# Optimization experiments

Measured on AMD Instinct MI355X. Metric: run time of the kernel, lower is better.

The kernel has to match this reference:

```python
import jax, jax.numpy as jnp
import numpy as np

NUM_HEADS = 16
HEAD_DIM = 64  # hidden_size / num_heads


def setup_inputs() -> dict:
    key = jax.random.key(0)
    ks = jax.random.split(key, 20)
    B, S, H, K = 16, 1024, 1024, 64
    d = {"hidden_states": jax.random.normal(ks[0], (B, S, H), jnp.float32)}
    i = 1
    for p in ("q", "k", "v", "o"):
        d["W" + p] = jax.random.normal(ks[i], (H, H), jnp.float32) * (1.0 / np.sqrt(H)); i += 1
        d["b" + p] = jax.random.normal(ks[i], (H,), jnp.float32) * 0.02; i += 1
        d["LM" + p] = jax.random.normal(ks[i], (H, K), jnp.float32) * (1.0 / np.sqrt(K)); i += 1
        d["RM" + p] = jax.random.normal(ks[i], (K, H), jnp.float32) * (1.0 / np.sqrt(H)); i += 1
        d["F" + p] = jnp.ones((H,), jnp.float32)
    d["task"] = 0
    return d


def _proj(x, W, b, LM, RM, F):
    # RG weight reconstruction: weight = LM @ RM + W  (task==0 branch)
    w = LM @ RM + W  # [h_out, h_in]
    y = jnp.einsum("bsi,oi->bso", x, w) + b
    return y * F  # SFG per-channel scaling


def reference(hidden_states, Wq, bq, LMq, RMq, Fq, Wk, bk, LMk, RMk, Fk,
              Wv, bv, LMv, RMv, Fv, Wo, bo, LMo, RMo, Fo, task):
    B, S, H = hidden_states.shape
    nh, hd = NUM_HEADS, HEAD_DIM
    q = _proj(hidden_states, Wq, bq, LMq, RMq, Fq).reshape(B, S, nh, hd)
    k = _proj(hidden_states, Wk, bk, LMk, RMk, Fk).reshape(B, S, nh, hd)
    v = _proj(hidden_states, Wv, bv, LMv, RMv, Fv).reshape(B, S, nh, hd)
    scores = jnp.einsum("bqhd,bkhd->bhqk", q, k) / np.sqrt(hd).astype(np.float32)
    probs = jax.nn.softmax(scores, axis=-1)  # attn_dropout rate = 0.0
    ctx = jnp.einsum("bhqk,bkhd->bqhd", probs, v).reshape(B, S, H)
    out = _proj(ctx, Wo, bo, LMo, RMo, Fo)  # proj_dropout rate = 0.0
    return out
```

## Files before the change

kernel.cpp:

```cpp
#include <hip/hip_runtime.h>
#include <cstdint>
#include <cstddef>

typedef short short8 __attribute__((ext_vector_type(8)));
typedef float f32x4 __attribute__((ext_vector_type(4)));
typedef float f32x16 __attribute__((ext_vector_type(16)));
typedef unsigned short us4 __attribute__((ext_vector_type(4)));

__device__ __forceinline__ unsigned short f2bf(float f) {
  unsigned int u = __float_as_uint(f);
  unsigned int r = (u + 0x7fffu + ((u >> 16) & 1u)) >> 16;
  return (unsigned short)r;
}
__device__ __forceinline__ float exp2_fast(float x) {
  return __builtin_amdgcn_exp2f(x);
}
__device__ __forceinline__ float max3f(float a, float b, float c) {
  return fmaxf(fmaxf(a, b), c);
}
__device__ __forceinline__ unsigned int cvt_pk_bf16(float a, float b) {
  unsigned int d;
  asm("v_cvt_pk_bf16_f32 %0, %1, %2" : "=v"(d) : "v"(a), "v"(b));
  return d;
}
__device__ __forceinline__ void permlane32_swap2(unsigned int& a, unsigned int& b) {
  asm("v_permlane32_swap_b32 %0, %1" : "+v"(a), "+v"(b));
}
__device__ __forceinline__ void gload_lds16(const void* g, void* l) {
  auto gp = reinterpret_cast<const __attribute__((address_space(1))) char*>(
      reinterpret_cast<uintptr_t>(g));
  auto lp = reinterpret_cast<__attribute__((address_space(3))) char*>(
      reinterpret_cast<uintptr_t>(l));
  __builtin_amdgcn_global_load_lds(gp, lp, 16, 0, 0);
}

__global__ __launch_bounds__(256) void prep_weights(
    const float* __restrict__ W, const float* __restrict__ bias,
    const float* __restrict__ LM, const float* __restrict__ RM,
    const float* __restrict__ F, float scale,
    unsigned short* __restrict__ Wout, float* __restrict__ bout) {
  const int o = blockIdx.x;
  const int tid = threadIdx.x;
  __shared__ float lm[64];
  if (tid < 64) lm[tid] = LM[o * 64 + tid];
  __syncthreads();
  const float f = F[o] * scale;
#pragma unroll
  for (int j = 0; j < 4; ++j) {
    const int i = tid + j * 256;
    float acc = W[o * 1024 + i];
#pragma unroll 16
    for (int k = 0; k < 64; ++k) acc = fmaf(lm[k], RM[k * 1024 + i], acc);
    Wout[o * 1024 + i] = f2bf(acc * f);
  }
  if (tid == 0) bout[o] = bias[o] * f;
}

__global__ __launch_bounds__(256) void cast_x(const float* __restrict__ x,
                                              unsigned short* __restrict__ y, int n4) {
  const int i = blockIdx.x * 256 + threadIdx.x;
  if (i >= n4) return;
  f32x4 v = *(const f32x4*)(x + (size_t)i * 4);
  us4 o;
  o[0] = f2bf(v[0]); o[1] = f2bf(v[1]); o[2] = f2bf(v[2]); o[3] = f2bf(v[3]);
  *(us4*)(y + (size_t)i * 4) = o;
}

template <int MODE>
__global__ __launch_bounds__(256) void gemm_bt(const unsigned short* __restrict__ A,
                                               const unsigned short* __restrict__ Bw,
                                               const float* __restrict__ bias,
                                               void* __restrict__ Cout,
                                               int M, int N, int K) {
  __shared__ unsigned short sA[2][128 * 64];
  __shared__ unsigned short sB[2][128 * 64];
  const int tid = threadIdx.x;
  const int w = tid >> 6;
  const int lane = tid & 63;
  const int quad = lane >> 4;
  const int ln = lane & 15;
  const int nbn = N >> 7;
  const int bid = (int)blockIdx.x;
  const int grp = bid / (nbn * 8);
  const int rem = bid - grp * (nbn * 8);
  const int bn = rem >> 3;
  const int bm = grp * 8 + (rem & 7);
  const int wm = w >> 1, wn = w & 1;

  f32x4 acc[4][4];
#pragma unroll
  for (int a = 0; a < 4; ++a)
#pragma unroll
    for (int b = 0; b < 4; ++b) acc[a][b] = (f32x4){0.f, 0.f, 0.f, 0.f};

  const size_t Kb = (size_t)K * 2;
  const char* Agb = (const char*)A + (size_t)bm * 128 * Kb;
  const char* Bgb = (const char*)Bw + (size_t)bn * 128 * Kb;
  const int sw = ln & 7;
  const int nt = K >> 6;

  auto stage = [&](int k0, int buf) {
    char* sAd = (char*)sA + buf * 16384;
    char* sBd = (char*)sB + buf * 16384;
#pragma unroll
    for (int i = 0; i < 4; ++i) {
      const int Lb = w * 4096 + i * 1024 + lane * 16;
      const int r = Lb >> 7;
      const int c = (Lb >> 4) & 7;
      const int cb = ((c ^ (r & 7)) * 16);
      gload_lds16(Agb + (size_t)r * Kb + (size_t)k0 * 2 + cb, sAd + Lb);
      gload_lds16(Bgb + (size_t)r * Kb + (size_t)k0 * 2 + cb, sBd + Lb);
    }
  };

  stage(0, 0);
  asm volatile("s_waitcnt vmcnt(0)" ::: "memory");
  __builtin_amdgcn_s_barrier();

  for (int t = 0; t < nt; ++t) {
    const int cur = t & 1;
    const char* sAc = (const char*)sA + cur * 16384;
    const char* sBc = (const char*)sB + cur * 16384;

    if (t + 1 < nt) stage((t + 1) << 6, cur ^ 1);

    short8 af[2][4], bfv[2][4];
#pragma unroll
    for (int kk = 0; kk < 2; ++kk)
#pragma unroll
      for (int t4 = 0; t4 < 4; ++t4) {
        const int ch = ((kk * 4 + quad) ^ sw) * 16;
        af[kk][t4]  = *(const short8*)(sAc + (wm * 64 + t4 * 16 + ln) * 128 + ch);
        bfv[kk][t4] = *(const short8*)(sBc + (wn * 64 + t4 * 16 + ln) * 128 + ch);
      }

    __builtin_amdgcn_s_setprio(1);
#pragma unroll
    for (int kk = 0; kk < 2; ++kk)
#pragma unroll
      for (int mt = 0; mt < 4; ++mt)
#pragma unroll
        for (int ntc = 0; ntc < 4; ++ntc)
          acc[mt][ntc] = __builtin_amdgcn_mfma_f32_16x16x32_bf16(af[kk][mt], bfv[kk][ntc], acc[mt][ntc], 0, 0, 0);
    __builtin_amdgcn_s_setprio(0);

    asm volatile("s_waitcnt vmcnt(0)" ::: "memory");
    __builtin_amdgcn_s_barrier();
    asm volatile("" ::: "memory");
  }

  if (MODE == 0) {
    unsigned short* out = (unsigned short*)Cout;
#pragma unroll
    for (int mt = 0; mt < 4; ++mt) {
#pragma unroll
      for (int ntc = 0; ntc < 4; ++ntc) {
        const int gn = bn * 128 + wn * 64 + ntc * 16 + ln;
        const float bv = bias[gn];
        const int pidx = gn >> 10, rem2 = gn & 1023;
        const int hh = rem2 >> 6, dd = rem2 & 63;
        const int gm0 = bm * 128 + wm * 64 + mt * 16 + quad * 4;
        const int bb = gm0 >> 10, ss0 = gm0 & 1023;
        if (pidx < 2) {
#pragma unroll
          for (int r = 0; r < 4; ++r) {
            const size_t off = ((((size_t)pidx * 16 + bb) * 16 + hh) * 1024 + (ss0 + r)) * 64 + dd;
            out[off] = f2bf(acc[mt][ntc][r] + bv);
          }
        } else {
          us4 pk;
#pragma unroll
          for (int r = 0; r < 4; ++r) pk[r] = f2bf(acc[mt][ntc][r] + bv);
          const size_t off = (size_t)2 * 16777216 +
                             (((size_t)(bb * 16 + hh) * 64 + dd) * 1024 + ss0);
          *(us4*)(out + off) = pk;
        }
      }
    }
  } else {
    float* out = (float*)Cout;
#pragma unroll
    for (int mt = 0; mt < 4; ++mt) {
#pragma unroll
      for (int ntc = 0; ntc < 4; ++ntc) {
        const int gn = bn * 128 + wn * 64 + ntc * 16 + ln;
        const float bv = bias[gn];
#pragma unroll
        for (int r = 0; r < 4; ++r) {
          const int gm = bm * 128 + wm * 64 + mt * 16 + quad * 4 + r;
          out[(size_t)gm * N + gn] = acc[mt][ntc][r] + bv;
        }
      }
    }
  }
}

__global__ __launch_bounds__(256) void attn(const unsigned short* __restrict__ Qb,
                                            const unsigned short* __restrict__ Kb_,
                                            const unsigned short* __restrict__ VTb,
                                            unsigned short* __restrict__ ctx) {
  __shared__ unsigned short sK[2][64 * 64];
  __shared__ unsigned short sVT[2][64 * 64];
  const int tid = threadIdx.x;
  const int w = tid >> 6, lane = tid & 63;
  const int col = lane & 31, hi = lane >> 5;
  const int sw7 = col & 7;
  const int bid = blockIdx.x;
  const int xcd = bid & 7, qt = (bid >> 3) & 7, sbh = bid >> 6;
  const int bh = xcd * 32 + sbh;
  const int b = bh >> 4, h = bh & 15;

  short8 bq[4];
  {
    const unsigned short* Qg =
        Qb + ((size_t)bh * 1024 + (size_t)qt * 128 + w * 32 + col) * 64 + hi * 8;
#pragma unroll
    for (int ks = 0; ks < 4; ++ks) bq[ks] = *(const short8*)(Qg + ks * 16);
  }

  f32x16 accO[2];
#pragma unroll
  for (int nt = 0; nt < 2; ++nt)
#pragma unroll
    for (int r = 0; r < 16; ++r) accO[nt][r] = 0.f;
  f32x16 zv;
#pragma unroll
  for (int r = 0; r < 16; ++r) zv[r] = 0.f;
  float mrun = -3e38f, lrun = 0.f;

  const char* Kbase = (const char*)Kb_ + (size_t)bh * 131072;
  const char* Vbase = (const char*)VTb + (size_t)bh * 131072;

  auto stage = [&](int kt, int buf) {
#pragma unroll
    for (int i = 0; i < 2; ++i) {
      const int Lb = w * 2048 + i * 1024 + lane * 16;
      const int r = Lb >> 7;
      const int c = (Lb >> 4) & 7;
      const int cb = ((c ^ (r & 7)) * 16);
      gload_lds16(Kbase + (size_t)kt * 8192 + (size_t)r * 128 + cb, (char*)sK[buf] + Lb);
      gload_lds16(Vbase + (size_t)kt * 128 + (size_t)r * 2048 + cb, (char*)sVT[buf] + Lb);
    }
  };

  stage(0, 0);

  for (int kt = 0; kt < 16; ++kt) {
    const int cur = kt & 1;
    const char* sKb = (const char*)sK[cur];
    const char* sVb = (const char*)sVT[cur];

    stage((kt + 1) & 15, cur ^ 1);
    asm volatile("s_waitcnt vmcnt(4)" ::: "memory");
    __builtin_amdgcn_s_barrier();
    asm volatile("" ::: "memory");

    f32x16 accS0, accS1;
    {
      const int ch = ((0 ^ (hi ^ sw7)) * 16) ^ 0;
      const int ch0 = ((hi ^ sw7) * 16);
      (void)ch;
      const short8 ak0 = *(const short8*)(sKb + (col)*128 + ch0);
      const short8 ak1 = *(const short8*)(sKb + (32 + col) * 128 + ch0);
      __builtin_amdgcn_s_setprio(1);
      accS0 = __builtin_amdgcn_mfma_f32_32x32x16_bf16(ak0, bq[0], zv, 0, 0, 0);
      accS1 = __builtin_amdgcn_mfma_f32_32x32x16_bf16(ak1, bq[0], zv, 0, 0, 0);
      __builtin_amdgcn_s_setprio(0);
    }
#pragma unroll
    for (int ks = 1; ks < 4; ++ks) {
      const int ch = (((2 * ks + hi) ^ sw7) * 16);
      const short8 ak0 = *(const short8*)(sKb + (col)*128 + ch);
      const short8 ak1 = *(const short8*)(sKb + (32 + col) * 128 + ch);
      __builtin_amdgcn_s_setprio(1);
      accS0 = __builtin_amdgcn_mfma_f32_32x32x16_bf16(ak0, bq[ks], accS0, 0, 0, 0);
      accS1 = __builtin_amdgcn_mfma_f32_32x32x16_bf16(ak1, bq[ks], accS1, 0, 0, 0);
      __builtin_amdgcn_s_setprio(0);
    }

    float t0 = max3f(accS0[0], accS0[1], accS0[2]);
    float t1 = max3f(accS0[3], accS0[4], accS0[5]);
    float t2 = max3f(accS0[6], accS0[7], accS0[8]);
    float t3 = max3f(accS0[9], accS0[10], accS0[11]);
    float t4 = max3f(accS0[12], accS0[13], accS0[14]);
    float t5 = max3f(accS0[15], accS1[0], accS1[1]);
    float t6 = max3f(accS1[2], accS1[3], accS1[4]);
    float t7 = max3f(accS1[5], accS1[6], accS1[7]);
    float t8 = max3f(accS1[8], accS1[9], accS1[10]);
    float t9 = max3f(accS1[11], accS1[12], accS1[13]);
    float ta = fmaxf(accS1[14], accS1[15]);
    float u0 = max3f(t0, t1, t2);
    float u1 = max3f(t3, t4, t5);
    float u2 = max3f(t6, t7, t8);
    float u3 = max3f(t9, ta, u0);
    float tmax = max3f(u1, u2, u3);
    tmax = fmaxf(tmax, __shfl_xor(tmax, 32));
    if (!__all(tmax <= mrun + 8.0f)) {
      const float mnew = fmaxf(mrun, tmax);
      const float alpha = exp2_fast(mrun - mnew);
      mrun = mnew;
      lrun *= alpha;
#pragma unroll
      for (int r = 0; r < 16; ++r) {
        const float ar = __shfl(alpha, (r & 3) + 8 * (r >> 2) + 4 * hi);
        accO[0][r] *= ar;
        accO[1][r] *= ar;
      }
    }
    const float m = mrun;

    float cs[2][2];
#pragma unroll
    for (int mt = 0; mt < 2; ++mt) {
#pragma unroll
      for (int c = 0; c < 2; ++c) {
        const f32x16& aS = (mt == 0) ? accS0 : accS1;
        const int r0 = c * 8;
        const float e0 = exp2_fast(aS[r0 + 0] - m);
        const float e1 = exp2_fast(aS[r0 + 1] - m);
        const float e2 = exp2_fast(aS[r0 + 2] - m);
        const float e3 = exp2_fast(aS[r0 + 3] - m);
        const float e4 = exp2_fast(aS[r0 + 4] - m);
        const float e5 = exp2_fast(aS[r0 + 5] - m);
        const float e6 = exp2_fast(aS[r0 + 6] - m);
        const float e7 = exp2_fast(aS[r0 + 7] - m);
        cs[mt][c] = ((e0 + e1) + (e2 + e3)) + ((e4 + e5) + (e6 + e7));
        unsigned int x = cvt_pk_bf16(e0, e1);
        unsigned int y = cvt_pk_bf16(e2, e3);
        unsigned int z = cvt_pk_bf16(e4, e5);
        unsigned int t = cvt_pk_bf16(e6, e7);
        permlane32_swap2(x, z);
        permlane32_swap2(y, t);
        union { unsigned int u[4]; short8 v; } pa;
        pa.u[0] = x; pa.u[1] = y; pa.u[2] = z; pa.u[3] = t;
        const int csl = mt * 4 + c * 2 + hi;
        const int ch = ((csl ^ sw7) * 16);
        const short8 bv0 = *(const short8*)(sVb + (col)*128 + ch);
        const short8 bv1 = *(const short8*)(sVb + (32 + col) * 128 + ch);
        __builtin_amdgcn_s_setprio(1);
        accO[0] = __builtin_amdgcn_mfma_f32_32x32x16_bf16(pa.v, bv0, accO[0], 0, 0, 0);
        accO[1] = __builtin_amdgcn_mfma_f32_32x32x16_bf16(pa.v, bv1, accO[1], 0, 0, 0);
        __builtin_amdgcn_s_setprio(0);
      }
    }
    lrun += (cs[0][0] + cs[0][1]) + (cs[1][0] + cs[1][1]);

    __builtin_amdgcn_s_barrier();
    asm volatile("" ::: "memory");
  }

  float lt = lrun + __shfl_xor(lrun, 32);
  const float inv = 1.0f / lt;
#pragma unroll
  for (int r = 0; r < 16; ++r) {
    const int qr = (r & 3) + 8 * (r >> 2) + 4 * hi;
    const float iv = __shfl(inv, qr);
    const int sg = qt * 128 + w * 32 + qr;
    const size_t base = ((size_t)(b * 1024 + sg)) * 1024 + h * 64;
    ctx[base + col] = f2bf(accO[0][r] * iv);
    ctx[base + 32 + col] = f2bf(accO[1][r] * iv);
  }
}

extern "C" void kernel_launch(void* const* d_in, const int* in_sizes, int n_in,
                              void* d_out, int out_size, void* d_ws, size_t ws_size,
                              hipStream_t stream) {
  const float* hs  = (const float*)d_in[0];
  const float* Wq  = (const float*)d_in[1];
  const float* bq  = (const float*)d_in[2];
  const float* LMq = (const float*)d_in[3];
  const float* RMq = (const float*)d_in[4];
  const float* Fq  = (const float*)d_in[5];
  const float* Wk  = (const float*)d_in[6];
  const float* bk  = (const float*)d_in[7];
  const float* LMk = (const float*)d_in[8];
  const float* RMk = (const float*)d_in[9];
  const float* Fk  = (const float*)d_in[10];
  const float* Wv  = (const float*)d_in[11];
  const float* bv  = (const float*)d_in[12];
  const float* LMv = (const float*)d_in[13];
  const float* RMv = (const float*)d_in[14];
  const float* Fv  = (const float*)d_in[15];
  const float* Wo  = (const float*)d_in[16];
  const float* bo  = (const float*)d_in[17];
  const float* LMo = (const float*)d_in[18];
  const float* RMo = (const float*)d_in[19];
  const float* Fo  = (const float*)d_in[20];

  char* p = (char*)d_ws;
  unsigned short* xbf  = (unsigned short*)p; p += (size_t)16384 * 1024 * 2;
  unsigned short* Wqkv = (unsigned short*)p; p += (size_t)3072 * 1024 * 2;
  unsigned short* Wob  = (unsigned short*)p; p += (size_t)1024 * 1024 * 2;
  float* bqkv = (float*)p; p += 3072 * 4;
  float* bob  = (float*)p; p += 1024 * 4;
  unsigned short* qkv = (unsigned short*)p; p += (size_t)3 * 16777216 * 2;
  unsigned short* ctx = (unsigned short*)p; p += (size_t)16777216 * 2;

  const float qscale = 0.125f * 1.4426950408889634f;

  cast_x<<<16384, 256, 0, stream>>>(hs, xbf, 16777216 / 4);
  prep_weights<<<1024, 256, 0, stream>>>(Wq, bq, LMq, RMq, Fq, qscale, Wqkv, bqkv);
  prep_weights<<<1024, 256, 0, stream>>>(Wk, bk, LMk, RMk, Fk, 1.0f, Wqkv + 1024 * 1024, bqkv + 1024);
  prep_weights<<<1024, 256, 0, stream>>>(Wv, bv, LMv, RMv, Fv, 1.0f, Wqkv + 2 * 1024 * 1024, bqkv + 2048);
  prep_weights<<<1024, 256, 0, stream>>>(Wo, bo, LMo, RMo, Fo, 1.0f, Wob, bob);

  gemm_bt<0><<<3072, 256, 0, stream>>>(xbf, Wqkv, bqkv, (void*)qkv, 16384, 3072, 1024);

  attn<<<2048, 256, 0, stream>>>(qkv, qkv + 16777216, qkv + 2 * 16777216, ctx);

  gemm_bt<1><<<1024, 256, 0, stream>>>(ctx, Wob, bob, d_out, 16384, 1024, 1024);
}
```

Baseline: 504.5 us.

## Enlarge GEMM tiles to 256x256 with 8 waves and interleaved load/MFMA schedule

Rewrites the projection GEMM to use 256x256 block tiles with 512 threads (8 waves, 2x4 layout), each wave computing 128x64. Global-to-LDS staging is prefetched two tiles ahead and split into phases interleaved with MFMA clusters, separated by barriers and sched_barrier. The goal is more data reuse per byte loaded and better overlap of memory traffic with matrix math. In exchange it uses 128KB of LDS per block, more accumulator registers and many more barriers, and the grid drops to 768 and 256 blocks, which may fill the GPU less evenly.

```diff
diff --git a/kernel.cpp b/kernel.cpp
--- a/kernel.cpp
+++ b/kernel.cpp
@@ -67,84 +67,131 @@
 }
 
 template <int MODE>
-__global__ __launch_bounds__(256) void gemm_bt(const unsigned short* __restrict__ A,
-                                               const unsigned short* __restrict__ Bw,
-                                               const float* __restrict__ bias,
-                                               void* __restrict__ Cout,
-                                               int M, int N, int K) {
-  __shared__ unsigned short sA[2][128 * 64];
-  __shared__ unsigned short sB[2][128 * 64];
+__global__ __launch_bounds__(512, 2) void gemm_bt(const unsigned short* __restrict__ A,
+                                                  const unsigned short* __restrict__ Bw,
+                                                  const float* __restrict__ bias,
+                                                  void* __restrict__ Cout,
+                                                  int M, int N, int K) {
+  __shared__ unsigned short sA[2][256 * 64];
+  __shared__ unsigned short sB[2][256 * 64];
   const int tid = threadIdx.x;
   const int w = tid >> 6;
   const int lane = tid & 63;
   const int quad = lane >> 4;
   const int ln = lane & 15;
-  const int nbn = N >> 7;
+  const int wm = w >> 2, wn = w & 3;
+  const int nbn = N >> 8;
   const int bid = (int)blockIdx.x;
-  const int grp = bid / (nbn * 8);
-  const int rem = bid - grp * (nbn * 8);
+  const int gsz = nbn * 8;
+  const int grp = bid / gsz;
+  const int rem = bid - grp * gsz;
   const int bn = rem >> 3;
   const int bm = grp * 8 + (rem & 7);
-  const int wm = w >> 1, wn = w & 1;
-
-  f32x4 acc[4][4];
-#pragma unroll
-  for (int a = 0; a < 4; ++a)
+
+  f32x4 acc[8][4];
+#pragma unroll
+  for (int a = 0; a < 8; ++a)
 #pragma unroll
     for (int b = 0; b < 4; ++b) acc[a][b] = (f32x4){0.f, 0.f, 0.f, 0.f};
 
   const size_t Kb = (size_t)K * 2;
-  const char* Agb = (const char*)A + (size_t)bm * 128 * Kb;
-  const char* Bgb = (const char*)Bw + (size_t)bn * 128 * Kb;
+  const char* Agb = (const char*)A + (size_t)bm * 256 * Kb;
+  const char* Bgb = (const char*)Bw + (size_t)bn * 256 * Kb;
   const int sw = ln & 7;
-  const int nt = K >> 6;
-
-  auto stage = [&](int k0, int buf) {
-    char* sAd = (char*)sA + buf * 16384;
-    char* sBd = (char*)sB + buf * 16384;
+  const int ntiles = K >> 6;
+
+  auto stageM = [&](const char* Gb, char* sDst, int t) {
 #pragma unroll
     for (int i = 0; i < 4; ++i) {
-      const int Lb = w * 4096 + i * 1024 + lane * 16;
+      const int Lb = i * 8192 + tid * 16;
       const int r = Lb >> 7;
       const int c = (Lb >> 4) & 7;
-      const int cb = ((c ^ (r & 7)) * 16);
-      gload_lds16(Agb + (size_t)r * Kb + (size_t)k0 * 2 + cb, sAd + Lb);
-      gload_lds16(Bgb + (size_t)r * Kb + (size_t)k0 * 2 + cb, sBd + Lb);
+      gload_lds16(Gb + (size_t)r * Kb + (size_t)t * 128 + ((c ^ (r & 7)) * 16), sDst + Lb);
     }
   };
 
-  stage(0, 0);
-  asm volatile("s_waitcnt vmcnt(0)" ::: "memory");
-  __builtin_amdgcn_s_barrier();
-
-  for (int t = 0; t < nt; ++t) {
-    const int cur = t & 1;
-    const char* sAc = (const char*)sA + cur * 16384;
-    const char* sBc = (const char*)sB + cur * 16384;
-
-    if (t + 1 < nt) stage((t + 1) << 6, cur ^ 1);
-
-    short8 af[2][4], bfv[2][4];
-#pragma unroll
-    for (int kk = 0; kk < 2; ++kk)
-#pragma unroll
-      for (int t4 = 0; t4 < 4; ++t4) {
-        const int ch = ((kk * 4 + quad) ^ sw) * 16;
-        af[kk][t4]  = *(const short8*)(sAc + (wm * 64 + t4 * 16 + ln) * 128 + ch);
-        bfv[kk][t4] = *(const short8*)(sBc + (wn * 64 + t4 * 16 + ln) * 128 + ch);
-      }
-
+  stageM(Agb, (char*)sA[0], 0);
+  stageM(Bgb, (char*)sB[0], 0);
+  if (ntiles > 1) {
+    stageM(Agb, (char*)sA[1], 1);
+    stageM(Bgb, (char*)sB[1], 1);
+  }
+
+  for (int t = 0; t < ntiles; ++t) {
+    const char* sAc = (const char*)sA + (t & 1) * 32768;
+    const char* sBc = (const char*)sB + (t & 1) * 32768;
+
+    if (t < ntiles - 1) {
+      asm volatile("s_waitcnt vmcnt(8)" ::: "memory");
+    } else {
+      asm volatile("s_waitcnt vmcnt(0)" ::: "memory");
+    }
+    __builtin_amdgcn_s_barrier();
+    asm volatile("" ::: "memory");
+
+    short8 af0[8], af1[8], bf0[4], bf1[4];
+
+#pragma unroll
+    for (int mt = 0; mt < 8; ++mt)
+      af0[mt] = *(const short8*)(sAc + (wm * 128 + mt * 16 + ln) * 128 + ((quad ^ sw) * 16));
+#pragma unroll
+    for (int nt = 0; nt < 4; ++nt)
+      bf0[nt] = *(const short8*)(sBc + (wn * 64 + nt * 16 + ln) * 128 + ((quad ^ sw) * 16));
+    __builtin_amdgcn_s_barrier();
+    asm volatile("s_waitcnt lgkmcnt(0)" ::: "memory");
+    __builtin_amdgcn_sched_barrier(0);
     __builtin_amdgcn_s_setprio(1);
 #pragma unroll
-    for (int kk = 0; kk < 2; ++kk)
-#pragma unroll
-      for (int mt = 0; mt < 4; ++mt)
-#pragma unroll
-        for (int ntc = 0; ntc < 4; ++ntc)
-          acc[mt][ntc] = __builtin_amdgcn_mfma_f32_16x16x32_bf16(af[kk][mt], bfv[kk][ntc], acc[mt][ntc], 0, 0, 0);
+    for (int mt = 0; mt < 8; ++mt) {
+      acc[mt][0] = __builtin_amdgcn_mfma_f32_16x16x32_bf16(af0[mt], bf0[0], acc[mt][0], 0, 0, 0);
+      acc[mt][1] = __builtin_amdgcn_mfma_f32_16x16x32_bf16(af0[mt], bf0[1], acc[mt][1], 0, 0, 0);
+    }
     __builtin_amdgcn_s_setprio(0);
-
-    asm volatile("s_waitcnt vmcnt(0)" ::: "memory");
+    __builtin_amdgcn_s_barrier();
+    asm volatile("" ::: "memory");
+
+#pragma unroll
+    for (int mt = 0; mt < 8; ++mt)
+      af1[mt] = *(const short8*)(sAc + (wm * 128 + mt * 16 + ln) * 128 + (((4 + quad) ^ sw) * 16));
+    __builtin_amdgcn_s_barrier();
+    asm volatile("s_waitcnt lgkmcnt(0)" ::: "memory");
+    __builtin_amdgcn_sched_barrier(0);
+    __builtin_amdgcn_s_setprio(1);
+#pragma unroll
+    for (int mt = 0; mt < 8; ++mt) {
+      acc[mt][2] = __builtin_amdgcn_mfma_f32_16x16x32_bf16(af0[mt], bf0[2], acc[mt][2], 0, 0, 0);
+      acc[mt][3] = __builtin_amdgcn_mfma_f32_16x16x32_bf16(af0[mt], bf0[3], acc[mt][3], 0, 0, 0);
+    }
+    __builtin_amdgcn_s_setprio(0);
+    __builtin_amdgcn_s_barrier();
+    asm volatile("" ::: "memory");
+
+#pragma unroll
+    for (int nt = 0; nt < 4; ++nt)
+      bf1[nt] = *(const short8*)(sBc + (wn * 64 + nt * 16 + ln) * 128 + (((4 + quad) ^ sw) * 16));
+    if (t + 2 < ntiles) stageM(Agb, (char*)sA + (t & 1) * 32768, t + 2);
+    __builtin_amdgcn_s_barrier();
+    asm volatile("s_waitcnt lgkmcnt(0)" ::: "memory");
+    __builtin_amdgcn_sched_barrier(0);
+    __builtin_amdgcn_s_setprio(1);
+#pragma unroll
+    for (int mt = 0; mt < 8; ++mt) {
+      acc[mt][0] = __builtin_amdgcn_mfma_f32_16x16x32_bf16(af1[mt], bf1[0], acc[mt][0], 0, 0, 0);
+      acc[mt][1] = __builtin_amdgcn_mfma_f32_16x16x32_bf16(af1[mt], bf1[1], acc[mt][1], 0, 0, 0);
+    }
+    __builtin_amdgcn_s_setprio(0);
+    __builtin_amdgcn_s_barrier();
+    asm volatile("" ::: "memory");
+
+    if (t + 2 < ntiles) stageM(Bgb, (char*)sB + (t & 1) * 32768, t + 2);
+    __builtin_amdgcn_s_barrier();
+    __builtin_amdgcn_s_setprio(1);
+#pragma unroll
+    for (int mt = 0; mt < 8; ++mt) {
+      acc[mt][2] = __builtin_amdgcn_mfma_f32_16x16x32_bf16(af1[mt], bf1[2], acc[mt][2], 0, 0, 0);
+      acc[mt][3] = __builtin_amdgcn_mfma_f32_16x16x32_bf16(af1[mt], bf1[3], acc[mt][3], 0, 0, 0);
+    }
+    __builtin_amdgcn_s_setprio(0);
     __builtin_amdgcn_s_barrier();
     asm volatile("" ::: "memory");
   }
@@ -152,14 +199,14 @@
   if (MODE == 0) {
     unsigned short* out = (unsigned short*)Cout;
 #pragma unroll
-    for (int mt = 0; mt < 4; ++mt) {
+    for (int mt = 0; mt < 8; ++mt) {
 #pragma unroll
       for (int ntc = 0; ntc < 4; ++ntc) {
-        const int gn = bn * 128 + wn * 64 + ntc * 16 + ln;
+        const int gn = bn * 256 + wn * 64 + ntc * 16 + ln;
         const float bv = bias[gn];
         const int pidx = gn >> 10, rem2 = gn & 1023;
         const int hh = rem2 >> 6, dd = rem2 & 63;
-        const int gm0 = bm * 128 + wm * 64 + mt * 16 + quad * 4;
+        const int gm0 = bm * 256 + wm * 128 + mt * 16 + quad * 4;
         const int bb = gm0 >> 10, ss0 = gm0 & 1023;
         if (pidx < 2) {
 #pragma unroll
@@ -180,14 +227,14 @@
   } else {
     float* out = (float*)Cout;
 #pragma unroll
-    for (int mt = 0; mt < 4; ++mt) {
+    for (int mt = 0; mt < 8; ++mt) {
 #pragma unroll
       for (int ntc = 0; ntc < 4; ++ntc) {
-        const int gn = bn * 128 + wn * 64 + ntc * 16 + ln;
+        const int gn = bn * 256 + wn * 64 + ntc * 16 + ln;
         const float bv = bias[gn];
 #pragma unroll
         for (int r = 0; r < 4; ++r) {
-          const int gm = bm * 128 + wm * 64 + mt * 16 + quad * 4 + r;
+          const int gm = bm * 256 + wm * 128 + mt * 16 + quad * 4 + r;
           out[(size_t)gm * N + gn] = acc[mt][ntc][r] + bv;
         }
       }
@@ -257,9 +304,7 @@
 
     f32x16 accS0, accS1;
     {
-      const int ch = ((0 ^ (hi ^ sw7)) * 16) ^ 0;
       const int ch0 = ((hi ^ sw7) * 16);
-      (void)ch;
       const short8 ak0 = *(const short8*)(sKb + (col)*128 + ch0);
       const short8 ak1 = *(const short8*)(sKb + (32 + col) * 128 + ch0);
       __builtin_amdgcn_s_setprio(1);
@@ -404,9 +449,9 @@
   prep_weights<<<1024, 256, 0, stream>>>(Wv, bv, LMv, RMv, Fv, 1.0f, Wqkv + 2 * 1024 * 1024, bqkv + 2048);
   prep_weights<<<1024, 256, 0, stream>>>(Wo, bo, LMo, RMo, Fo, 1.0f, Wob, bob);
 
-  gemm_bt<0><<<3072, 256, 0, stream>>>(xbf, Wqkv, bqkv, (void*)qkv, 16384, 3072, 1024);
+  gemm_bt<0><<<768, 512, 0, stream>>>(xbf, Wqkv, bqkv, (void*)qkv, 16384, 3072, 1024);
 
   attn<<<2048, 256, 0, stream>>>(qkv, qkv + 16777216, qkv + 2 * 16777216, ctx);
 
-  gemm_bt<1><<<1024, 256, 0, stream>>>(ctx, Wob, bob, d_out, 16384, 1024, 1024);
-}
+  gemm_bt<1><<<256, 512, 0, stream>>>(ctx, Wob, bob, d_out, 16384, 1024, 1024);
+}
```

Result: faster. 478.7 us (-5.1%).
